# Optimization experiments

Hardware: AMD Instinct MI355X
Metric: run time of the kernel (lower is better)

## Reference

```python
import jax, jax.numpy as jnp
import numpy as np

D_MODEL = 512
DFF = 2048
E = 8
K = 2
B, N = 2, 2048


def setup_inputs() -> dict:
    key = jax.random.key(0)
    ks = jax.random.split(key, 6)
    x = jax.random.normal(ks[0], (B, N, D_MODEL), dtype=jnp.float32)
    # router: nn.Linear(d_model, E, bias=False), init normal(std=0.01), weight [E, d]
    router_w = jax.random.normal(ks[1], (E, D_MODEL), dtype=jnp.float32) * 0.01
    # expert linear1.weight [dff, d], linear2.weight [d, dff], xavier-uniform; biases zero in torch init,
    # but use small random biases so the backward test exercises their grads meaningfully.
    lim1 = float(np.sqrt(6.0 / (D_MODEL + DFF)))
    w1_all = jax.random.uniform(ks[2], (E, DFF, D_MODEL), minval=-lim1, maxval=lim1, dtype=jnp.float32)
    w2_all = jax.random.uniform(ks[3], (E, D_MODEL, DFF), minval=-lim1, maxval=lim1, dtype=jnp.float32)
    b1_all = jax.random.normal(ks[4], (E, DFF), dtype=jnp.float32) * 0.01
    b2_all = jax.random.normal(ks[5], (E, D_MODEL), dtype=jnp.float32) * 0.01
    return {"x": x, "router_w": router_w, "w1_all": w1_all, "b1_all": b1_all,
            "w2_all": w2_all, "b2_all": b2_all}


def reference(x, router_w, w1_all, b1_all, w2_all, b2_all):
    Bb, Nn, C = x.shape
    L = Bb * Nn
    x_flat = x.reshape(L, C)

    # Router: logits -> softmax -> top-k -> renormalized weights
    router_logits = x_flat @ router_w.T                      # [L, E]
    router_probs = jax.nn.softmax(router_logits, axis=-1)
    expert_weights, expert_indices = jax.lax.top_k(router_probs, K)  # [L, K]
    expert_weights = expert_weights / (jnp.sum(expert_weights, axis=-1, keepdims=True) + 1e-9)

    # Dense per-expert MLP (same math as per-token gathered bmm; dropout in eval = identity)
    h = jax.nn.relu(jnp.einsum('lc,efc->lef', x_flat, w1_all) + b1_all[None])  # [L, E, dff]
    out_all = jnp.einsum('lef,ecf->lec', h, w2_all) + b2_all[None]             # [L, E, C]

    # Gather selected experts' outputs and combine
    out_sel = jnp.take_along_axis(out_all, expert_indices[:, :, None], axis=1)  # [L, K, C]
    final = jnp.sum(out_sel * expert_weights[:, :, None], axis=1)               # [L, C]
    return final.reshape(Bb, Nn, C)
```

## Files before the change

kernel.cpp:

```cpp
#include <hip/hip_runtime.h>

#define D_MODEL 512
#define DFF 2048
#define NEXP 8
#define LTOK 4096
#define NPAIR 8192
#define PMAX 9216
#define MAXT 72

#define HD_COUNTS 0
#define HD_CURSOR 8
#define HD_OFF    16
#define HD_NTILES 25
#define HD_DONE   26
#define HD_TILE_E 32
#define HD_TILE_R 112

typedef __attribute__((ext_vector_type(8))) short bf16x8;
typedef __attribute__((ext_vector_type(4))) float f32x4;

__device__ __forceinline__ unsigned short f2bf(float f){
  unsigned u = __builtin_bit_cast(unsigned, f);
  u += 0x7fffu + ((u>>16)&1u);
  return (unsigned short)(u>>16);
}

template<int N> __device__ __forceinline__ void wait_vm(){
  if constexpr (N==8)      asm volatile("s_waitcnt vmcnt(8)" ::: "memory");
  else if constexpr (N==6) asm volatile("s_waitcnt vmcnt(6)" ::: "memory");
  else                     asm volatile("s_waitcnt vmcnt(0)" ::: "memory");
}
#define RAW_BARRIER() asm volatile("s_barrier" ::: "memory")

__global__ void router_top2(const float* __restrict__ x, const float* __restrict__ rw,
                            int* __restrict__ pair_e, float* __restrict__ pair_w,
                            int* __restrict__ hdr){
  if (blockIdx.x==0) hdr[threadIdx.x] = 0;
  int t = blockIdx.x*4 + (threadIdx.x>>6);
  int l = threadIdx.x & 63;
  const float* xr = x + (size_t)t*D_MODEL;
  float xv[8];
  #pragma unroll
  for (int j=0;j<8;j++) xv[j] = xr[j*64+l];
  double lg[NEXP];
  #pragma unroll
  for (int e=0;e<NEXP;e++){
    const float* we = rw + e*D_MODEL;
    double s = 0.0;
    #pragma unroll
    for (int j=0;j<8;j++) s += (double)xv[j] * (double)we[j*64+l];
    #pragma unroll
    for (int off=32; off; off>>=1) s += __shfl_xor(s, off);
    lg[e] = s;
  }
  if (l==0){
    double mx = lg[0];
    #pragma unroll
    for (int e=1;e<NEXP;e++) if (lg[e]>mx) mx = lg[e];
    double p[NEXP], sum = 0.0;
    #pragma unroll
    for (int e=0;e<NEXP;e++){ p[e] = exp(lg[e]-mx); sum += p[e]; }
    #pragma unroll
    for (int e=0;e<NEXP;e++) p[e] /= sum;
    int i0 = 0;
    for (int e=1;e<NEXP;e++) if (p[e] > p[i0]) i0 = e;
    int i1 = (i0==0) ? 1 : 0;
    for (int e=0;e<NEXP;e++){ if (e==i0) continue; if (p[e] > p[i1]) i1 = e; }
    double s2 = p[i0] + p[i1] + 1e-9;
    pair_e[2*t]   = i0;  pair_e[2*t+1] = i1;
    pair_w[2*t]   = (float)(p[i0]/s2);
    pair_w[2*t+1] = (float)(p[i1]/s2);
  }
}

__global__ void convw_kernel(const float* __restrict__ w1, const float* __restrict__ w2,
                             unsigned short* __restrict__ w1b, unsigned short* __restrict__ w2b){
  int id = blockIdx.x*256 + threadIdx.x;
  const int per = NEXP*DFF*D_MODEL/8;
  const float* src; unsigned short* dst; int k;
  if (id < per){ src = w1; dst = w1b; k = id; }
  else         { src = w2; dst = w2b; k = id - per; }
  const float4* s = (const float4*)(src + (size_t)k*8);
  float4 a = s[0], b = s[1];
  uint4 o;
  o.x = (unsigned)f2bf(a.x) | ((unsigned)f2bf(a.y)<<16);
  o.y = (unsigned)f2bf(a.z) | ((unsigned)f2bf(a.w)<<16);
  o.z = (unsigned)f2bf(b.x) | ((unsigned)f2bf(b.y)<<16);
  o.w = (unsigned)f2bf(b.z) | ((unsigned)f2bf(b.w)<<16);
  *(uint4*)(dst + (size_t)k*8) = o;
}

__global__ void countplan_kernel(const int* __restrict__ pair_e, int* __restrict__ hdr,
                                 int* __restrict__ gtk){
  __shared__ int cnt[NEXP];
  int tid = threadIdx.x;
  if (tid < NEXP) cnt[tid] = 0;
  __syncthreads();
  int base = blockIdx.x*1024;
  #pragma unroll
  for (int i=0;i<4;i++) atomicAdd(&cnt[pair_e[base + i*256 + tid]], 1);
  __syncthreads();
  if (tid < NEXP){
    int old = atomicAdd(&hdr[HD_COUNTS+tid], cnt[tid]);
    (void)old;
  }
  for (int i = blockIdx.x*256 + tid; i < PMAX; i += 8*256) gtk[i] = -1;
  __syncthreads();
  if (tid==0){
    int done = atomicAdd(&hdr[HD_DONE], 1);
    if (done == 7){
      int off=0, nt=0;
      for (int e=0;e<NEXP;e++){
        hdr[HD_OFF+e] = off;
        int c = atomicAdd(&hdr[HD_COUNTS+e], 0);
        int tiles = (c+127)>>7;
        for (int i=0;i<tiles;i++){ hdr[HD_TILE_E+nt]=e; hdr[HD_TILE_R+nt]=off+(i<<7); nt++; }
        off += tiles<<7;
      }
      hdr[HD_OFF+NEXP]=off;
      hdr[HD_NTILES]=nt;
    }
  }
}

__global__ void assign_gather_kernel(const int* __restrict__ pair_e, int* __restrict__ hdr,
                                     int* __restrict__ gtk, int* __restrict__ pr,
                                     const float* __restrict__ x,
                                     unsigned short* __restrict__ xg){
  __shared__ int cnt[NEXP];
  __shared__ int base[NEXP];
  __shared__ int rowbuf[256];
  int tid = threadIdx.x;
  if (tid < NEXP) cnt[tid] = 0;
  __syncthreads();
  int id = blockIdx.x*256 + tid;
  int e = pair_e[id];
  int myrank = atomicAdd(&cnt[e], 1);
  __syncthreads();
  if (tid < NEXP) base[tid] = atomicAdd(&hdr[HD_CURSOR+tid], cnt[tid]);
  __syncthreads();
  int row = hdr[HD_OFF+e] + base[e] + myrank;
  gtk[row] = id;
  pr[id]   = row;
  rowbuf[tid] = row;
  __syncthreads();
  int grp = tid>>6, sub = tid&63;
  int base0 = blockIdx.x*256;
  for (int p = grp; p < 256; p += 4){
    int r = rowbuf[p];
    int t = (base0 + p)>>1;
    const float4* s = (const float4*)(x + (size_t)t*D_MODEL + sub*8);
    float4 a = s[0], b = s[1];
    uint4 o;
    o.x = (unsigned)f2bf(a.x) | ((unsigned)f2bf(a.y)<<16);
    o.y = (unsigned)f2bf(a.z) | ((unsigned)f2bf(a.w)<<16);
    o.z = (unsigned)f2bf(b.x) | ((unsigned)f2bf(b.y)<<16);
    o.w = (unsigned)f2bf(b.z) | ((unsigned)f2bf(b.w)<<16);
    *(uint4*)(xg + (size_t)r*D_MODEL + sub*8) = o;
  }
}

template<int MT, int NDIM, int KDIM, int MODE>
__global__ __launch_bounds__(256,2) void gemm2p(
    const unsigned short* __restrict__ A,
    const unsigned short* __restrict__ Bw,
    const float* __restrict__ bias,
    unsigned short* __restrict__ outH,
    float* __restrict__ outO,
    const float* __restrict__ pair_w,
    const int* __restrict__ hdr,
    const int* __restrict__ gtk)
{
  constexpr int NT_N = NDIM/128;
  constexpr int MAXM = (MT==128) ? MAXT : 2*MAXT;
  constexpr int NWG  = MAXM*NT_N;
  constexpr int WC   = (MT==128) ? 64 : 32;
  constexpr int FN   = WC/16;
  constexpr int LPT  = MT/32 + 4;
  constexpr int ABYT = MT*128;
  constexpr int NTK  = KDIM/64;

  __shared__ __align__(16) unsigned short As[2*MT*64];
  __shared__ __align__(16) unsigned short Bs[2*128*64];

  int wg  = blockIdx.x;
  int swz = (wg & 7)*(NWG/8) + (wg >> 3);
  int m   = swz / NT_N;
  int n0  = (swz % NT_N) << 7;

  int ntiles = hdr[HD_NTILES];
  int e, row0;
  if constexpr (MT==128){
    if (m >= ntiles) return;
    e = hdr[HD_TILE_E+m];  row0 = hdr[HD_TILE_R+m];
  } else {
    if (m >= 2*ntiles) return;
    e = hdr[HD_TILE_E+(m>>1)];  row0 = hdr[HD_TILE_R+(m>>1)] + ((m&1)<<6);
  }

  int tid = threadIdx.x;
  int w = tid>>6, l = tid&63;
  int wm = (MT==128) ? (w>>1) : 0;
  int wn = (MT==128) ? (w&1)  : w;

  const unsigned short* Ag = A  + (size_t)row0*KDIM;
  const unsigned short* Bg = Bw + (size_t)e*NDIM*KDIM + (size_t)n0*KDIM;

  f32x4 acc[4][FN];
  f32x4 zz = {0.f,0.f,0.f,0.f};
  #pragma unroll
  for (int i=0;i<4;i++)
    #pragma unroll
    for (int j=0;j<FN;j++) acc[i][j] = zz;

  int srow = (w<<3) + (l>>3);
  int c8   = l&7;
  char* AsB = (char*)As;
  char* BsB = (char*)Bs;

  auto stage = [&](int b, int kt){
    #pragma unroll
    for (int i=0;i<MT/32;i++){
      int r  = i*32 + srow;
      int sc = (c8 ^ (r&7))*8;
      const unsigned short* ga = Ag + (size_t)r*KDIM + kt*64 + sc;
      int ldso = b*ABYT + i*4096 + w*1024 + l*16;
      __builtin_amdgcn_global_load_lds((const __attribute__((address_space(1))) void*)ga,
                                       (__attribute__((address_space(3))) void*)(AsB + ldso), 16, 0, 0);
    }
    #pragma unroll
    for (int i=0;i<4;i++){
      int r  = i*32 + srow;
      int sc = (c8 ^ (r&7))*8;
      const unsigned short* gb = Bg + (size_t)r*KDIM + kt*64 + sc;
      int ldso = b*16384 + i*4096 + w*1024 + l*16;
      __builtin_amdgcn_global_load_lds((const __attribute__((address_space(1))) void*)gb,
                                       (__attribute__((address_space(3))) void*)(BsB + ldso), 16, 0, 0);
    }
  };

  auto compute = [&](int b){
    #pragma unroll
    for (int kk=0;kk<2;kk++){
      bf16x8 av[4], bv[FN];
      #pragma unroll
      for (int mi=0;mi<4;mi++){
        int r  = (wm<<6) + (mi<<4) + (l&15);
        int ch = ((kk<<2) + (l>>4)) ^ (r&7);
        av[mi] = *(const bf16x8*)(AsB + b*ABYT + r*128 + ch*16);
      }
      #pragma unroll
      for (int ni=0;ni<FN;ni++){
        int r  = wn*WC + (ni<<4) + (l&15);
        int ch = ((kk<<2) + (l>>4)) ^ (r&7);
        bv[ni] = *(const bf16x8*)(BsB + b*16384 + r*128 + ch*16);
      }
      #pragma unroll
      for (int mi=0;mi<4;mi++)
        #pragma unroll
        for (int ni=0;ni<FN;ni++)
          acc[mi][ni] = __builtin_amdgcn_mfma_f32_16x16x32_bf16(av[mi], bv[ni], acc[mi][ni], 0,0,0);
    }
  };

  stage(0, 0);
  int cur = 0;
  for (int kt=0; kt<NTK-1; ++kt){
    stage(cur^1, kt+1);
    wait_vm<LPT>();
    RAW_BARRIER();
    compute(cur);
    asm volatile("s_waitcnt lgkmcnt(0)" ::: "memory");
    RAW_BARRIER();
    cur ^= 1;
  }
  wait_vm<0>();
  RAW_BARRIER();
  compute(cur);

  int lc = l&15, lq = l>>4;
  #pragma unroll
  for (int ni=0;ni<FN;ni++){
    int col = n0 + wn*WC + (ni<<4) + lc;
    float bcol = bias[e*NDIM + col];
    #pragma unroll
    for (int mi=0;mi<4;mi++){
      int rbase = row0 + (wm<<6) + (mi<<4) + lq*4;
      #pragma unroll
      for (int q=0;q<4;q++){
        int gr = rbase + q;
        float v = acc[mi][ni][q] + bcol;
        if (MODE==0){
          v = v>0.f ? v : 0.f;
          outH[(size_t)gr*NDIM + col] = f2bf(v);
        } else {
          int tk = gtk[gr];
          if (tk>=0){
            float wgt = pair_w[tk];
            atomicAdd(&outO[(size_t)(tk>>1)*D_MODEL + col], wgt*v);
          }
        }
      }
    }
  }
}

__global__ __launch_bounds__(256,3) void gemm2s_k(
    const unsigned short* __restrict__ A,
    const unsigned short* __restrict__ Bw,
    float* __restrict__ P,
    const int* __restrict__ hdr)
{
  constexpr int NWG = 2*MAXT*4*2;
  constexpr int NTK = 16;
  __shared__ __align__(16) unsigned short As[2*64*64];
  __shared__ __align__(16) unsigned short Bs[2*128*64];

  int wg  = blockIdx.x;
  int swz = (wg & 7)*(NWG/8) + (wg >> 3);
  int m   = swz >> 3;
  int nt  = (swz >> 1) & 3;
  int kh  = swz & 1;

  if (m >= 2*hdr[HD_NTILES]) return;
  int e    = hdr[HD_TILE_E+(m>>1)];
  int row0 = hdr[HD_TILE_R+(m>>1)] + ((m&1)<<6);
  int n0   = nt << 7;

  int tid = threadIdx.x;
  int w = tid>>6, l = tid&63;

  const unsigned short* Ag = A  + (size_t)row0*DFF + (size_t)kh*1024;
  const unsigned short* Bg = Bw + (size_t)e*D_MODEL*DFF + (size_t)n0*DFF + (size_t)kh*1024;

  f32x4 acc[4][2];
  f32x4 zz = {0.f,0.f,0.f,0.f};
  #pragma unroll
  for (int i=0;i<4;i++)
    #pragma unroll
    for (int j=0;j<2;j++) acc[i][j] = zz;

  int srow = (w<<3) + (l>>3);
  int c8   = l&7;
  char* AsB = (char*)As;
  char* BsB = (char*)Bs;

  auto stage = [&](int b, int kt){
    #pragma unroll
    for (int i=0;i<2;i++){
      int r  = i*32 + srow;
      int sc = (c8 ^ (r&7))*8;
      const unsigned short* ga = Ag + (size_t)r*DFF + kt*64 + sc;
      int ldso = b*8192 + i*4096 + w*1024 + l*16;
      __builtin_amdgcn_global_load_lds((const __attribute__((address_space(1))) void*)ga,
                                       (__attribute__((address_space(3))) void*)(AsB + ldso), 16, 0, 0);
    }
    #pragma unroll
    for (int i=0;i<4;i++){
      int r  = i*32 + srow;
      int sc = (c8 ^ (r&7))*8;
      const unsigned short* gb = Bg + (size_t)r*DFF + kt*64 + sc;
      int ldso = b*16384 + i*4096 + w*1024 + l*16;
      __builtin_amdgcn_global_load_lds((const __attribute__((address_space(1))) void*)gb,
                                       (__attribute__((address_space(3))) void*)(BsB + ldso), 16, 0, 0);
    }
  };

  auto compute = [&](int b){
    #pragma unroll
    for (int kk=0;kk<2;kk++){
      bf16x8 av[4], bv[2];
      #pragma unroll
      for (int mi=0;mi<4;mi++){
        int r  = (mi<<4) + (l&15);
        int ch = ((kk<<2) + (l>>4)) ^ (r&7);
        av[mi] = *(const bf16x8*)(AsB + b*8192 + r*128 + ch*16);
      }
      #pragma unroll
      for (int ni=0;ni<2;ni++){
        int r  = (w<<5) + (ni<<4) + (l&15);
        int ch = ((kk<<2) + (l>>4)) ^ (r&7);
        bv[ni] = *(const bf16x8*)(BsB + b*16384 + r*128 + ch*16);
      }
      #pragma unroll
      for (int mi=0;mi<4;mi++)
        #pragma unroll
        for (int ni=0;ni<2;ni++)
          acc[mi][ni] = __builtin_amdgcn_mfma_f32_16x16x32_bf16(av[mi], bv[ni], acc[mi][ni], 0,0,0);
    }
  };

  stage(0, 0);
  int cur = 0;
  for (int kt=0; kt<NTK-1; ++kt){
    stage(cur^1, kt+1);
    wait_vm<6>();
    RAW_BARRIER();
    compute(cur);
    asm volatile("s_waitcnt lgkmcnt(0)" ::: "memory");
    RAW_BARRIER();
    cur ^= 1;
  }
  wait_vm<0>();
  RAW_BARRIER();
  compute(cur);

  float* Pk = P + (size_t)kh*PMAX*D_MODEL;
  int lc = l&15, lq = l>>4;
  #pragma unroll
  for (int ni=0;ni<2;ni++){
    int col = n0 + (w<<5) + (ni<<4) + lc;
    #pragma unroll
    for (int mi=0;mi<4;mi++){
      int rbase = row0 + (mi<<4) + lq*4;
      #pragma unroll
      for (int q=0;q<4;q++)
        Pk[(size_t)(rbase+q)*D_MODEL + col] = acc[mi][ni][q];
    }
  }
}

__global__ void combine_kernel(const float* __restrict__ P, const int* __restrict__ pr,
                               const int* __restrict__ pair_e, const float* __restrict__ pair_w,
                               const float* __restrict__ b2, float* __restrict__ out){
  int id = blockIdx.x*256 + threadIdx.x;
  int t = id>>7, c = (id&127)*4;
  int r0 = pr[2*t], r1 = pr[2*t+1];
  int e0 = pair_e[2*t], e1 = pair_e[2*t+1];
  float w0 = pair_w[2*t], w1 = pair_w[2*t+1];
  const float* P1 = P + (size_t)PMAX*D_MODEL;
  float4 a0 = *(const float4*)(P  + (size_t)r0*D_MODEL + c);
  float4 a1 = *(const float4*)(P1 + (size_t)r0*D_MODEL + c);
  float4 c0 = *(const float4*)(P  + (size_t)r1*D_MODEL + c);
  float4 c1 = *(const float4*)(P1 + (size_t)r1*D_MODEL + c);
  float4 bb0 = *(const float4*)(b2 + (size_t)e0*D_MODEL + c);
  float4 bb1 = *(const float4*)(b2 + (size_t)e1*D_MODEL + c);
  float4 r;
  r.x = w0*(a0.x+a1.x+bb0.x) + w1*(c0.x+c1.x+bb1.x);
  r.y = w0*(a0.y+a1.y+bb0.y) + w1*(c0.y+c1.y+bb1.y);
  r.z = w0*(a0.z+a1.z+bb0.z) + w1*(c0.z+c1.z+bb1.z);
  r.w = w0*(a0.w+a1.w+bb0.w) + w1*(c0.w+c1.w+bb1.w);
  *(float4*)(out + (size_t)t*D_MODEL + c) = r;
}

extern "C" void kernel_launch(void* const* d_in, const int* in_sizes, int n_in,
                              void* d_out, int out_size, void* d_ws, size_t ws_size,
                              hipStream_t stream){
  const float* x  = (const float*)d_in[0];
  const float* rw = (const float*)d_in[1];
  const float* w1 = (const float*)d_in[2];
  const float* b1 = (const float*)d_in[3];
  const float* w2 = (const float*)d_in[4];
  const float* b2 = (const float*)d_in[5];
  float* out = (float*)d_out;

  const size_t OFF_HDR  = 0;
  const size_t OFF_PE   = 1024;
  const size_t OFF_PW   = 66560;
  const size_t OFF_GTK  = 99328;
  const size_t OFF_PR   = 143360;
  const size_t OFF_XG   = 180224;
  const size_t OFF_W1B  = OFF_XG  + (size_t)PMAX*D_MODEL*2;
  const size_t OFF_W2B  = OFF_W1B + (size_t)NEXP*DFF*D_MODEL*2;
  const size_t OFF_H    = OFF_W2B + (size_t)NEXP*DFF*D_MODEL*2;
  const size_t WS_BASE  = OFF_H   + (size_t)PMAX*DFF*2;
  const size_t OFF_P    = WS_BASE;
  const size_t WS_SPLIT = OFF_P + (size_t)2*PMAX*D_MODEL*4;
  if (ws_size < WS_BASE) return;
  bool split = (ws_size >= WS_SPLIT);

  char* ws = (char*)d_ws;
  int*   hdr    = (int*)(ws + OFF_HDR);
  int*   pair_e = (int*)(ws + OFF_PE);
  float* pair_w = (float*)(ws + OFF_PW);
  int*   gtk    = (int*)(ws + OFF_GTK);
  int*   pr     = (int*)(ws + OFF_PR);
  unsigned short* xg  = (unsigned short*)(ws + OFF_XG);
  unsigned short* w1b = (unsigned short*)(ws + OFF_W1B);
  unsigned short* w2b = (unsigned short*)(ws + OFF_W2B);
  unsigned short* h   = (unsigned short*)(ws + OFF_H);
  float*          P   = (float*)(ws + OFF_P);

  router_top2<<<LTOK/4, 256, 0, stream>>>(x, rw, pair_e, pair_w, hdr);
  convw_kernel<<<8192, 256, 0, stream>>>(w1, w2, w1b, w2b);
  countplan_kernel<<<NPAIR/1024, 256, 0, stream>>>(pair_e, hdr, gtk);
  assign_gather_kernel<<<NPAIR/256, 256, 0, stream>>>(pair_e, hdr, gtk, pr, x, xg);
  gemm2p<128, DFF, D_MODEL, 0><<<MAXT*16, 256, 0, stream>>>(xg, w1b, b1, h, nullptr, nullptr, hdr, gtk);
  if (split){
    gemm2s_k<<<2*MAXT*4*2, 256, 0, stream>>>(h, w2b, P, hdr);
    combine_kernel<<<(LTOK*128)/256, 256, 0, stream>>>(P, pr, pair_e, pair_w, b2, out);
  } else {
    hipMemsetAsync(out, 0, (size_t)LTOK*D_MODEL*sizeof(float), stream);
    gemm2p<64, D_MODEL, DFF, 1><<<2*MAXT*4, 256, 0, stream>>>(h, w2b, b2, nullptr, out, pair_w, hdr, gtk);
  }
}
```

Before: 128.4 us.

## Fuse count/plan and assign/gather into one grid-synced prep kernel

Merges the counting/planning kernel and the assign/gather kernel into a single kernel. Its 32 blocks sync through an atomic counter spin-wait so every block can compute expert offsets before gathering rows. The gtk init moves into the router kernel, and the b2 bias add moves from the combine kernel into the split-K GEMM epilogue. The aim is to cut one launch and some combine-kernel loads. In exchange the spin barrier relies on all 32 blocks being co-resident, and the bias is added once per row in the kh==0 partial.

```diff
diff --git a/kernel.cpp b/kernel.cpp
--- a/kernel.cpp
+++ b/kernel.cpp
@@ -34,8 +34,9 @@
 
 __global__ void router_top2(const float* __restrict__ x, const float* __restrict__ rw,
                             int* __restrict__ pair_e, float* __restrict__ pair_w,
-                            int* __restrict__ hdr){
+                            int* __restrict__ hdr, int* __restrict__ gtk){
   if (blockIdx.x==0) hdr[threadIdx.x] = 0;
+  for (int i = blockIdx.x*256 + threadIdx.x; i < PMAX; i += (LTOK/4)*256) gtk[i] = -1;
   int t = blockIdx.x*4 + (threadIdx.x>>6);
   int l = threadIdx.x & 63;
   const float* xr = x + (size_t)t*D_MODEL;
@@ -90,45 +91,12 @@
   *(uint4*)(dst + (size_t)k*8) = o;
 }
 
-__global__ void countplan_kernel(const int* __restrict__ pair_e, int* __restrict__ hdr,
-                                 int* __restrict__ gtk){
+__global__ void prep_all(const int* __restrict__ pair_e, int* __restrict__ hdr,
+                         int* __restrict__ gtk, int* __restrict__ pr,
+                         const float* __restrict__ x, unsigned short* __restrict__ xg){
   __shared__ int cnt[NEXP];
-  int tid = threadIdx.x;
-  if (tid < NEXP) cnt[tid] = 0;
-  __syncthreads();
-  int base = blockIdx.x*1024;
-  #pragma unroll
-  for (int i=0;i<4;i++) atomicAdd(&cnt[pair_e[base + i*256 + tid]], 1);
-  __syncthreads();
-  if (tid < NEXP){
-    int old = atomicAdd(&hdr[HD_COUNTS+tid], cnt[tid]);
-    (void)old;
-  }
-  for (int i = blockIdx.x*256 + tid; i < PMAX; i += 8*256) gtk[i] = -1;
-  __syncthreads();
-  if (tid==0){
-    int done = atomicAdd(&hdr[HD_DONE], 1);
-    if (done == 7){
-      int off=0, nt=0;
-      for (int e=0;e<NEXP;e++){
-        hdr[HD_OFF+e] = off;
-        int c = atomicAdd(&hdr[HD_COUNTS+e], 0);
-        int tiles = (c+127)>>7;
-        for (int i=0;i<tiles;i++){ hdr[HD_TILE_E+nt]=e; hdr[HD_TILE_R+nt]=off+(i<<7); nt++; }
-        off += tiles<<7;
-      }
-      hdr[HD_OFF+NEXP]=off;
-      hdr[HD_NTILES]=nt;
-    }
-  }
-}
-
-__global__ void assign_gather_kernel(const int* __restrict__ pair_e, int* __restrict__ hdr,
-                                     int* __restrict__ gtk, int* __restrict__ pr,
-                                     const float* __restrict__ x,
-                                     unsigned short* __restrict__ xg){
-  __shared__ int cnt[NEXP];
-  __shared__ int base[NEXP];
+  __shared__ int bbase[NEXP];
+  __shared__ int off[NEXP+1];
   __shared__ int rowbuf[256];
   int tid = threadIdx.x;
   if (tid < NEXP) cnt[tid] = 0;
@@ -137,9 +105,22 @@
   int e = pair_e[id];
   int myrank = atomicAdd(&cnt[e], 1);
   __syncthreads();
-  if (tid < NEXP) base[tid] = atomicAdd(&hdr[HD_CURSOR+tid], cnt[tid]);
+  if (tid < NEXP) bbase[tid] = atomicAdd(&hdr[HD_CURSOR+tid], cnt[tid]);
   __syncthreads();
-  int row = hdr[HD_OFF+e] + base[e] + myrank;
+  __threadfence();
+  if (tid==0){
+    atomicAdd(&hdr[HD_DONE], 1);
+    while (atomicAdd(&hdr[HD_DONE], 0) < 32) __builtin_amdgcn_s_sleep(8);
+    int o = 0;
+    for (int e2=0;e2<NEXP;e2++){
+      off[e2] = o;
+      int c = atomicAdd(&hdr[HD_CURSOR+e2], 0);
+      o += ((c+127)>>7)<<7;
+    }
+    off[NEXP] = o;
+  }
+  __syncthreads();
+  int row = off[e] + bbase[e] + myrank;
   gtk[row] = id;
   pr[id]   = row;
   rowbuf[tid] = row;
@@ -157,6 +138,17 @@
     o.z = (unsigned)f2bf(b.x) | ((unsigned)f2bf(b.y)<<16);
     o.w = (unsigned)f2bf(b.z) | ((unsigned)f2bf(b.w)<<16);
     *(uint4*)(xg + (size_t)r*D_MODEL + sub*8) = o;
+  }
+  if (blockIdx.x==0 && tid==0){
+    int nt = 0;
+    for (int e2=0;e2<NEXP;e2++){
+      hdr[HD_OFF+e2] = off[e2];
+      int c = atomicAdd(&hdr[HD_CURSOR+e2], 0);
+      int tiles = (c+127)>>7;
+      for (int i=0;i<tiles;i++){ hdr[HD_TILE_E+nt]=e2; hdr[HD_TILE_R+nt]=off[e2]+(i<<7); nt++; }
+    }
+    hdr[HD_OFF+NEXP] = off[NEXP];
+    hdr[HD_NTILES]   = nt;
   }
 }
 
@@ -308,6 +300,7 @@
 __global__ __launch_bounds__(256,3) void gemm2s_k(
     const unsigned short* __restrict__ A,
     const unsigned short* __restrict__ Bw,
+    const float* __restrict__ b2,
     float* __restrict__ P,
     const int* __restrict__ hdr)
 {
@@ -410,36 +403,33 @@
   #pragma unroll
   for (int ni=0;ni<2;ni++){
     int col = n0 + (w<<5) + (ni<<4) + lc;
+    float bcol = (kh==0) ? b2[e*D_MODEL + col] : 0.f;
     #pragma unroll
     for (int mi=0;mi<4;mi++){
       int rbase = row0 + (mi<<4) + lq*4;
       #pragma unroll
       for (int q=0;q<4;q++)
-        Pk[(size_t)(rbase+q)*D_MODEL + col] = acc[mi][ni][q];
+        Pk[(size_t)(rbase+q)*D_MODEL + col] = acc[mi][ni][q] + bcol;
     }
   }
 }
 
 __global__ void combine_kernel(const float* __restrict__ P, const int* __restrict__ pr,
-                               const int* __restrict__ pair_e, const float* __restrict__ pair_w,
-                               const float* __restrict__ b2, float* __restrict__ out){
+                               const float* __restrict__ pair_w, float* __restrict__ out){
   int id = blockIdx.x*256 + threadIdx.x;
   int t = id>>7, c = (id&127)*4;
   int r0 = pr[2*t], r1 = pr[2*t+1];
-  int e0 = pair_e[2*t], e1 = pair_e[2*t+1];
   float w0 = pair_w[2*t], w1 = pair_w[2*t+1];
   const float* P1 = P + (size_t)PMAX*D_MODEL;
   float4 a0 = *(const float4*)(P  + (size_t)r0*D_MODEL + c);
   float4 a1 = *(const float4*)(P1 + (size_t)r0*D_MODEL + c);
   float4 c0 = *(const float4*)(P  + (size_t)r1*D_MODEL + c);
   float4 c1 = *(const float4*)(P1 + (size_t)r1*D_MODEL + c);
-  float4 bb0 = *(const float4*)(b2 + (size_t)e0*D_MODEL + c);
-  float4 bb1 = *(const float4*)(b2 + (size_t)e1*D_MODEL + c);
   float4 r;
-  r.x = w0*(a0.x+a1.x+bb0.x) + w1*(c0.x+c1.x+bb1.x);
-  r.y = w0*(a0.y+a1.y+bb0.y) + w1*(c0.y+c1.y+bb1.y);
-  r.z = w0*(a0.z+a1.z+bb0.z) + w1*(c0.z+c1.z+bb1.z);
-  r.w = w0*(a0.w+a1.w+bb0.w) + w1*(c0.w+c1.w+bb1.w);
+  r.x = w0*(a0.x+a1.x) + w1*(c0.x+c1.x);
+  r.y = w0*(a0.y+a1.y) + w1*(c0.y+c1.y);
+  r.z = w0*(a0.z+a1.z) + w1*(c0.z+c1.z);
+  r.w = w0*(a0.w+a1.w) + w1*(c0.w+c1.w);
   *(float4*)(out + (size_t)t*D_MODEL + c) = r;
 }
 
@@ -481,14 +471,13 @@
   unsigned short* h   = (unsigned short*)(ws + OFF_H);
   float*          P   = (float*)(ws + OFF_P);
 
-  router_top2<<<LTOK/4, 256, 0, stream>>>(x, rw, pair_e, pair_w, hdr);
+  router_top2<<<LTOK/4, 256, 0, stream>>>(x, rw, pair_e, pair_w, hdr, gtk);
   convw_kernel<<<8192, 256, 0, stream>>>(w1, w2, w1b, w2b);
-  countplan_kernel<<<NPAIR/1024, 256, 0, stream>>>(pair_e, hdr, gtk);
-  assign_gather_kernel<<<NPAIR/256, 256, 0, stream>>>(pair_e, hdr, gtk, pr, x, xg);
+  prep_all<<<NPAIR/256, 256, 0, stream>>>(pair_e, hdr, gtk, pr, x, xg);
   gemm2p<128, DFF, D_MODEL, 0><<<MAXT*16, 256, 0, stream>>>(xg, w1b, b1, h, nullptr, nullptr, hdr, gtk);
   if (split){
-    gemm2s_k<<<2*MAXT*4*2, 256, 0, stream>>>(h, w2b, P, hdr);
-    combine_kernel<<<(LTOK*128)/256, 256, 0, stream>>>(P, pr, pair_e, pair_w, b2, out);
+    gemm2s_k<<<2*MAXT*4*2, 256, 0, stream>>>(h, w2b, b2, P, hdr);
+    combine_kernel<<<(LTOK*128)/256, 256, 0, stream>>>(P, pr, pair_w, out);
   } else {
     hipMemsetAsync(out, 0, (size_t)LTOK*D_MODEL*sizeof(float), stream);
     gemm2p<64, D_MODEL, DFF, 1><<<2*MAXT*4, 256, 0, stream>>>(h, w2b, b2, nullptr, out, pair_w, hdr, gtk);
```

After: 128.5 us. About the same (+0.1%).
